# Performance work log

Hardware: AMD Instinct MI355X
Metric: run time of the kernel (lower is better)

Reference implementation:

```python
import jax, jax.numpy as jnp
import numpy as np

B, NQ, T, C = 16, 1024, 2048, 4
DIM, CDIM, H, DH = 512, 256, 1, 128
INNER = H * DH


def _rotate_half(x):
    # pairs interleaved: (..., d*2) -> (-x_odd, x_even) interleaved, matching einops '(d r)' with r=2
    x2 = x.reshape(x.shape[:-1] + (-1, 2))
    a, b = x2[..., 0], x2[..., 1]
    return jnp.stack((-b, a), axis=-1).reshape(x.shape)


def _apply_rotary(freqs, x):
    # freqs: (b, n, d) -> broadcast over heads; x: (b, h, n, d)
    f = freqs[:, None, :, :]
    return x * jnp.cos(f) + _rotate_half(x) * jnp.sin(f)


def _layernorm(x, w, b, eps=1e-5):
    mu = jnp.mean(x, axis=-1, keepdims=True)
    var = jnp.var(x, axis=-1, keepdims=True)
    return (x - mu) * jax.lax.rsqrt(var + eps) * w + b


def setup_inputs() -> dict:
    key = jax.random.key(0)
    ks = jax.random.split(key, 8)
    return dict(
        x_query=jax.random.normal(ks[0], (NQ, DIM), jnp.float32),
        x_context=jax.random.normal(ks[1], (B, T, C, CDIM), jnp.float32),
        rotary_time_emb_query=jax.random.normal(ks[2], (B, NQ, DH), jnp.float32),
        rotary_time_emb_context=jax.random.normal(ks[3], (B, T * C, DH), jnp.float32),
        context_mask=jax.random.randint(ks[4], (B, T), 0, 2) > 0,
        ln_q_w=jnp.ones((DIM,), jnp.float32), ln_q_b=jnp.zeros((DIM,), jnp.float32),
        ln_c_w=jnp.ones((CDIM,), jnp.float32), ln_c_b=jnp.zeros((CDIM,), jnp.float32),
        w_q=jax.random.normal(ks[5], (INNER, DIM), jnp.float32) / np.float32(np.sqrt(DIM)),
        w_kv=jax.random.normal(ks[6], (2 * INNER, CDIM), jnp.float32) / np.float32(np.sqrt(CDIM)),
        w_o=jax.random.normal(ks[7], (DIM, INNER), jnp.float32) / np.float32(np.sqrt(INNER)),
        b_o=jnp.zeros((DIM,), jnp.float32),
    )


def reference(x_query, x_context, rotary_time_emb_query, rotary_time_emb_context,
              context_mask, ln_q_w, ln_q_b, ln_c_w, ln_c_b, w_q, w_kv, w_o, b_o):
    b = x_context.shape[0]
    xq = _layernorm(x_query, ln_q_w, ln_q_b)                      # (NQ, DIM)
    xc = _layernorm(x_context, ln_c_w, ln_c_b)                    # (B, T, C, CDIM)
    q = xq @ w_q.T                                                # (NQ, INNER)
    q = jnp.broadcast_to(q[None], (b,) + q.shape)                 # (B, NQ, INNER)
    kv = xc @ w_kv.T                                              # (B, T, C, 2*INNER)
    k, v = jnp.split(kv, 2, axis=-1)
    k = k.reshape(b, -1, k.shape[-1])                             # (B, T*C, INNER)
    v = v.reshape(b, -1, v.shape[-1])

    def to_heads(t):  # 'b n (h d) -> b h n d'
        return t.reshape(t.shape[0], t.shape[1], H, DH).transpose(0, 2, 1, 3)

    q, k, v = to_heads(q), to_heads(k), to_heads(v)
    q = _apply_rotary(rotary_time_emb_query, q)
    k = _apply_rotary(rotary_time_emb_context, k)
    v = _apply_rotary(rotary_time_emb_context, v)                 # rotate_value=True

    # kv_mask: 'b n -> b 1 1 n' then tiled x4 along last dim (as in source)
    mask = jnp.tile(context_mask[:, None, None, :], (1, 1, 1, 4)) # (B,1,1,4T)
    scale = np.float32(1.0 / np.sqrt(DH))
    logits = jnp.einsum('bhqd,bhkd->bhqk', q, k) * scale
    logits = jnp.where(mask, logits, jnp.float32(-1e30))
    attn = jax.nn.softmax(logits, axis=-1)
    out = jnp.einsum('bhqk,bhkd->bhqd', attn, v)                  # (B,H,NQ,DH)
    out = _apply_rotary(-rotary_time_emb_query, out)              # un-rotate values
    out = out.mean(axis=2)                                        # (B, H, DH)
    return out @ w_o.T + b_o                                      # (B, H, DIM)
```

## Files before the change

### kernel.cpp

```cpp
#include <hip/hip_runtime.h>
#include <hip/hip_bf16.h>


#define DEV static __device__ __forceinline__

typedef __attribute__((ext_vector_type(4))) float f32x4;
typedef __attribute__((ext_vector_type(8))) short s16x8;
typedef __attribute__((ext_vector_type(4))) unsigned u32x4;

constexpr int NB   = 16;
constexpr int NQ   = 1024;
constexpr int SC   = 8192;
constexpr int DIM  = 512;
constexpr int CDIM = 256;
constexpr int DH   = 128;
constexpr int VTR  = 144;
constexpr int VTILE = VTR*64;

DEV short f2bf(float x){
  unsigned u = __builtin_bit_cast(unsigned, x);
  unsigned r = (u + 0x7FFFu + ((u >> 16) & 1u)) >> 16;
  return (short)r;
}

DEV unsigned pk2(float a, float b){
  unsigned short ua = __builtin_bit_cast(unsigned short, __float2bfloat16(a));
  unsigned short ub = __builtin_bit_cast(unsigned short, __float2bfloat16(b));
  return (unsigned)ua | ((unsigned)ub << 16);
}

DEV f32x4 mfma16(s16x8 a, s16x8 b, f32x4 c){
  return __builtin_amdgcn_mfma_f32_16x16x32_bf16(a, b, c, 0, 0, 0);
}

DEV void gload16(const void* g, void* l){
  __builtin_amdgcn_global_load_lds(
      (const __attribute__((address_space(1))) void*)g,
      (__attribute__((address_space(3))) void*)l, 16, 0, 0);
}

DEV s16x8 pexch(int ia0, int ia1, bool hi, unsigned L0, unsigned H0, unsigned L1, unsigned H1){
  int aL0 = __builtin_amdgcn_ds_bpermute(ia0, (int)L0);
  int aL1 = __builtin_amdgcn_ds_bpermute(ia0, (int)L1);
  int aH0 = __builtin_amdgcn_ds_bpermute(ia0, (int)H0);
  int aH1 = __builtin_amdgcn_ds_bpermute(ia0, (int)H1);
  int bL0 = __builtin_amdgcn_ds_bpermute(ia1, (int)L0);
  int bL1 = __builtin_amdgcn_ds_bpermute(ia1, (int)L1);
  int bH0 = __builtin_amdgcn_ds_bpermute(ia1, (int)H0);
  int bH1 = __builtin_amdgcn_ds_bpermute(ia1, (int)H1);
  u32x4 r;
  r[0] = (unsigned)(hi ? aL1 : aL0);
  r[1] = (unsigned)(hi ? aH1 : aH0);
  r[2] = (unsigned)(hi ? bL1 : bL0);
  r[3] = (unsigned)(hi ? bH1 : bH0);
  return __builtin_bit_cast(s16x8, r);
}

__global__ void k_cvtw(const float* __restrict__ wq, const float* __restrict__ wkv,
                       short* __restrict__ wqb, short* __restrict__ wkvb){
  int i = blockIdx.x * 256 + threadIdx.x;
  if(i < 128*512) wqb[i]  = f2bf(wq[i]);
  if(i < 256*256) wkvb[i] = f2bf(wkv[i]);
}

__global__ void k_mask(const unsigned char* __restrict__ raw, unsigned* __restrict__ bits){
  const int b = blockIdx.x, t = threadIdx.x;
  int nz = 0;
  for(int i = t; i < 8192; i += 256){
    unsigned w = ((const unsigned*)raw)[i];
    if(w & 0xFFFFFF00u) nz = 1;
  }
  int any = __syncthreads_or(nz);
  bool isInt = (any == 0);
  if(t < 64){
    unsigned out = 0;
    if(isInt){
      const int* p = (const int*)raw + (b*2048 + t*32);
      for(int j = 0; j < 32; j++) out |= (unsigned)(p[j] != 0) << j;
    } else {
      const unsigned char* p = raw + (b*2048 + t*32);
      for(int j = 0; j < 32; j++) out |= (unsigned)(p[j] != 0) << j;
    }
    bits[b*64 + t] = out;
  }
}

__global__ void k_vrow(const unsigned* __restrict__ bits, short* __restrict__ Vt){
  int b = blockIdx.y;
  int s = blockIdx.x * 256 + threadIdx.x;
  unsigned w = bits[b*64 + ((s & 2047) >> 5)];
  short v = ((w >> (s & 31)) & 1u) ? (short)0x3F80 : (short)0;
  Vt[(((size_t)b*128 + (s >> 6))*VTR + 128)*64 + (s & 63)] = v;
}

__global__ __launch_bounds__(256) void k_stats(const float* __restrict__ xc,
                                               float* __restrict__ MU, float* __restrict__ RS){
  const size_t row = (size_t)blockIdx.x * 16 + (threadIdx.x >> 4);
  const int cl = (threadIdx.x & 15) * 16;
  const float* rp = xc + row * CDIM + cl;
  float s = 0.f, sq = 0.f;
  #pragma unroll
  for(int i = 0; i < 4; i++){
    f32x4 a = *(const f32x4*)(rp + i*4);
    #pragma unroll
    for(int j = 0; j < 4; j++){ s += a[j]; sq += a[j]*a[j]; }
  }
  #pragma unroll
  for(int o = 8; o > 0; o >>= 1){ s += __shfl_xor(s, o); sq += __shfl_xor(sq, o); }
  if((threadIdx.x & 15) == 0){
    float m = s * (1.f/CDIM);
    MU[row] = m;
    RS[row] = rsqrtf(sq * (1.f/CDIM) - m*m + 1e-5f);
  }
}

__global__ __launch_bounds__(256) void k_qproj(const float* __restrict__ xq,
                                               const float* __restrict__ lnw, const float* __restrict__ lnb,
                                               const short* __restrict__ wqb, float* __restrict__ Q0){
  const int wid = threadIdx.x >> 6, lane = threadIdx.x & 63;
  const int g = lane >> 4, li = lane & 15;
  const int row0 = blockIdx.x * 64 + wid * 16;

  float mean = 0.f, rstd = 0.f;
  #pragma unroll
  for(int r = 0; r < 16; r++){
    const float* rp = xq + (row0 + r) * DIM;
    f32x4 a = *(const f32x4*)(rp + lane*8);
    f32x4 b = *(const f32x4*)(rp + lane*8 + 4);
    float s = 0.f, sq = 0.f;
    #pragma unroll
    for(int i = 0; i < 4; i++){ s += a[i] + b[i]; sq += a[i]*a[i] + b[i]*b[i]; }
    #pragma unroll
    for(int o = 32; o > 0; o >>= 1){ s += __shfl_xor(s, o); sq += __shfl_xor(sq, o); }
    if(li == r){
      mean = s / DIM;
      float var = sq / DIM - mean*mean;
      rstd = rsqrtf(var + 1e-5f);
    }
  }

  f32x4 acc[8];
  #pragma unroll
  for(int n = 0; n < 8; n++) acc[n] = f32x4{0.f,0.f,0.f,0.f};

  for(int kc = 0; kc < 16; kc++){
    int kd = kc*32 + g*8;
    const float* rp = xq + (row0 + li)*DIM + kd;
    f32x4 a0 = *(const f32x4*)rp;
    f32x4 a1 = *(const f32x4*)(rp + 4);
    f32x4 w0 = *(const f32x4*)(lnw + kd), w1 = *(const f32x4*)(lnw + kd + 4);
    f32x4 b0 = *(const f32x4*)(lnb + kd), b1 = *(const f32x4*)(lnb + kd + 4);
    s16x8 af;
    #pragma unroll
    for(int i = 0; i < 4; i++){
      af[i]   = f2bf((a0[i] - mean)*rstd*w0[i] + b0[i]);
      af[i+4] = f2bf((a1[i] - mean)*rstd*w1[i] + b1[i]);
    }
    #pragma unroll
    for(int n = 0; n < 8; n++){
      s16x8 bf = *(const s16x8*)(wqb + (n*16 + li)*DIM + kd);
      acc[n] = mfma16(af, bf, acc[n]);
    }
  }
  #pragma unroll
  for(int n = 0; n < 8; n++)
    #pragma unroll
    for(int r = 0; r < 4; r++){
      int m = row0 + g*4 + r;
      Q0[m*DH + n*16 + li] = acc[n][r];
    }
}

__global__ __launch_bounds__(512, 4) void k_kvproj(const float* __restrict__ xc,
                                                   const float* __restrict__ lnw, const float* __restrict__ lnb,
                                                   const short* __restrict__ wkvb, const float* __restrict__ rc,
                                                   const unsigned* __restrict__ bits,
                                                   const float* __restrict__ MU, const float* __restrict__ RS,
                                                   short* __restrict__ Kd, short* __restrict__ Vt){
  __shared__ __align__(16) short Klds[128][136];
  __shared__ __align__(16) short Vtlds[128][136];
  const int wid = threadIdx.x >> 6, lane = threadIdx.x & 63;
  const int g = lane >> 4, li = lane & 15;
  const int wk = wid & 3;
  const int isV = wid >> 2;
  const int b = blockIdx.y;
  const int s0 = blockIdx.x * 128;
  const int ws0 = s0 + wk * 32;

  float mean_s[2], rstd_s[2];
  #pragma unroll
  for(int sub = 0; sub < 2; sub++){
    size_t row = (size_t)b*SC + ws0 + sub*16 + li;
    mean_s[sub] = MU[row];
    rstd_s[sub] = RS[row];
  }

  f32x4 acc[8][2];
  #pragma unroll
  for(int n = 0; n < 8; n++){ acc[n][0] = f32x4{0.f,0.f,0.f,0.f}; acc[n][1] = f32x4{0.f,0.f,0.f,0.f}; }

  for(int kc = 0; kc < 8; kc++){
    int kd = kc*32 + g*8;
    f32x4 w0 = *(const f32x4*)(lnw + kd), w1 = *(const f32x4*)(lnw + kd + 4);
    f32x4 b0 = *(const f32x4*)(lnb + kd), b1 = *(const f32x4*)(lnb + kd + 4);
    s16x8 af[2];
    #pragma unroll
    for(int sub = 0; sub < 2; sub++){
      const float* rp = xc + ((size_t)b*SC + ws0 + sub*16 + li)*CDIM + kd;
      f32x4 a0 = *(const f32x4*)rp;
      f32x4 a1 = *(const f32x4*)(rp + 4);
      float mn = mean_s[sub], rs = rstd_s[sub];
      #pragma unroll
      for(int i = 0; i < 4; i++){
        af[sub][i]   = f2bf((a0[i]-mn)*rs*w0[i] + b0[i]);
        af[sub][i+4] = f2bf((a1[i]-mn)*rs*w1[i] + b1[i]);
      }
    }
    #pragma unroll
    for(int ntl = 0; ntl < 8; ntl++){
      const int nt = isV*8 + ntl;
      s16x8 bf = *(const s16x8*)(wkvb + (nt*16 + li)*CDIM + kd);
      acc[ntl][0] = mfma16(af[0], bf, acc[ntl][0]);
      acc[ntl][1] = mfma16(af[1], bf, acc[ntl][1]);
    }
  }

  if(isV == 0){
    #pragma unroll
    for(int ntl = 0; ntl < 8; ntl++)
      #pragma unroll
      for(int sub = 0; sub < 2; sub++)
        #pragma unroll
        for(int r = 0; r < 4; r++){
          int srow = wk*32 + sub*16 + g*4 + r;
          int d = ntl*16 + li;
          float f = rc[((size_t)b*SC + s0 + srow)*DH + d];
          float sn, cs; __sincosf(f, &sn, &cs);
          float kv = acc[ntl][sub][r];
          float kp = __shfl_xor(kv, 1);
          float ky = (d & 1) ? (kv*cs + kp*sn) : (kv*cs - kp*sn);
          Klds[srow][d] = f2bf(ky);
        }
  } else {
    #pragma unroll
    for(int ntl = 0; ntl < 8; ntl++)
      #pragma unroll
      for(int sub = 0; sub < 2; sub++)
        #pragma unroll
        for(int r = 0; r < 4; r++){
          int srow = wk*32 + sub*16 + g*4 + r;
          int d = ntl*16 + li;
          float f = rc[((size_t)b*SC + s0 + srow)*DH + d];
          float sn, cs; __sincosf(f, &sn, &cs);
          float vv = acc[ntl][sub][r];
          float vp = __shfl_xor(vv, 1);
          float vy = (d & 1) ? (vv*cs + vp*sn) : (vv*cs - vp*sn);
          Vtlds[d][srow] = f2bf(vy);
        }
  }
  __syncthreads();
  for(int c = threadIdx.x; c < 2048; c += 512){
    int row = c >> 4, col = (c & 15) * 8;
    s16x8 kv = *(const s16x8*)&Klds[row][col];
    *(s16x8*)(Kd + ((size_t)b*SC + s0 + row)*DH + col) = kv;
    s16x8 vv = *(const s16x8*)&Vtlds[row][col];
    int sa = s0 + col;
    unsigned w = bits[b*64 + ((sa & 2047) >> 5)];
    unsigned mb = (w >> (sa & 31)) & 0xFFu;
    #pragma unroll
    for(int j = 0; j < 8; j++) if(!((mb >> j) & 1u)) vv[j] = 0;
    *(s16x8*)(Vt + (((size_t)b*128 + (sa >> 6))*VTR + row)*64 + (sa & 63)) = vv;
  }
}

__global__ __launch_bounds__(512, 4) void k_attn(const float* __restrict__ Q0, const float* __restrict__ rq,
                                                 const short* __restrict__ Kd, const short* __restrict__ Vt,
                                                 float* __restrict__ AOp, float* __restrict__ ML){
  __shared__ __align__(16) short Kbuf[2][64*128];
  __shared__ __align__(16) short Vbuf[2][VTR*64];
  const int wid = threadIdx.x >> 6, lane = threadIdx.x & 63;
  const int g = lane >> 4, li = lane & 15;
  const int xcd = blockIdx.x & 7, ii = blockIdx.x >> 3;
  const int b  = xcd*2 + (ii >> 5);
  const int kq = (ii >> 3) & 3;
  const int qt = ii & 7;
  const int qw0 = qt*128 + wid*16;
  constexpr float C2 = 0.08838834764831845f * 1.4426950408889634f;

  s16x8 qf[4];
  {
    int qrow = qw0 + li;
    #pragma unroll
    for(int c = 0; c < 4; c++){
      int d0 = c*32 + g*8;
      const float* qp = Q0 + qrow*DH + d0;
      const float* fp = rq + ((size_t)b*NQ + qrow)*DH + d0;
      f32x4 x0 = *(const f32x4*)qp,     x1 = *(const f32x4*)(qp+4);
      f32x4 f0 = *(const f32x4*)fp,     f1 = *(const f32x4*)(fp+4);
      float xs[8] = {x0[0],x0[1],x0[2],x0[3],x1[0],x1[1],x1[2],x1[3]};
      float fs[8] = {f0[0],f0[1],f0[2],f0[3],f1[0],f1[1],f1[2],f1[3]};
      #pragma unroll
      for(int i = 0; i < 4; i++){
        float se, ce, so, co;
        __sincosf(fs[2*i],   &se, &ce);
        __sincosf(fs[2*i+1], &so, &co);
        qf[c][2*i]   = f2bf((xs[2*i]*ce   - xs[2*i+1]*se) * C2);
        qf[c][2*i+1] = f2bf((xs[2*i+1]*co + xs[2*i]*so) * C2);
      }
    }
  }

  float mrun = -1e30f;
  f32x4 acc[9];
  #pragma unroll
  for(int dt = 0; dt < 9; dt++) acc[dt] = f32x4{0.f,0.f,0.f,0.f};

  const char* Kg = (const char*)(Kd + ((size_t)b*SC + kq*2048)*DH);
  const char* Vg = (const char*)(Vt + ((size_t)b*128 + kq*32)*VTILE);

  const int ia0 = (((lane >> 4) & 1) * 32 + li) << 2;
  const int ia1 = ia0 + 64;
  const bool hi = (g >= 2);

  #define STAGE(bufi, t) do{                                                   \
    const char* Ksrc = Kg + (size_t)(t)*64*256;                                \
    _Pragma("unroll")                                                          \
    for(int j = 0; j < 2; j++){                                                \
      int rp = wid*8 + j*4 + (lane >> 4);                                      \
      int bi = ((lane & 15)*16) ^ ((rp & 7) << 4);                             \
      gload16(Ksrc + rp*256 + bi, &Kbuf[bufi][(wid*8 + j*4)*128]);             \
    }                                                                          \
    const char* Vsrc = Vg + (size_t)(t)*VTILE*2;                               \
    _Pragma("unroll")                                                          \
    for(int j = 0; j < 2; j++){                                                \
      int rp = wid*16 + j*8 + (lane >> 3);                                     \
      int bi = ((lane & 7)*16) ^ ((rp & 7) << 4);                              \
      gload16(Vsrc + rp*128 + bi, &Vbuf[bufi][(wid*16 + j*8)*64]);             \
    }                                                                          \
    if(wid < 2){                                                               \
      int rp = 128 + wid*8 + (lane >> 3);                                      \
      int bi = ((lane & 7)*16) ^ ((rp & 7) << 4);                              \
      gload16(Vsrc + rp*128 + bi, &Vbuf[bufi][(128 + wid*8)*64]);              \
    }                                                                          \
  }while(0)

  STAGE(0, 0);
  __syncthreads();

  for(int t = 0; t < 32; ++t){
    const int cur = t & 1;
    if(t < 31) STAGE(cur^1, t+1);

    f32x4 st[4];
    __builtin_amdgcn_s_setprio(1);
    #pragma unroll
    for(int ks = 0; ks < 4; ks++){
      s16x8 kf[4];
      #pragma unroll
      for(int c = 0; c < 4; c++){
        int row = ks*16 + li;
        int off = row*256 + ((c*64 + g*16) ^ ((row & 7) << 4));
        kf[c] = *(const s16x8*)((const char*)&Kbuf[cur][0] + off);
      }
      f32x4 s = f32x4{0.f,0.f,0.f,0.f};
      #pragma unroll
      for(int c = 0; c < 4; c++) s = mfma16(kf[c], qf[c], s);
      st[ks] = s;
    }
    __builtin_amdgcn_s_setprio(0);

    s16x8 pf[2];
    {
      float mt = -1e30f;
      #pragma unroll
      for(int ks = 0; ks < 4; ks++)
        #pragma unroll
        for(int r = 0; r < 4; r++) mt = fmaxf(mt, st[ks][r]);
      mt = fmaxf(mt, __shfl_xor(mt, 16));
      mt = fmaxf(mt, __shfl_xor(mt, 32));
      if(__any(mt > mrun + 3.0f)){
        float mnew = fmaxf(mrun, mt);
        float a = exp2f(mrun - mnew);
        mrun = mnew;
        #pragma unroll
        for(int dt = 0; dt < 9; dt++) acc[dt] = acc[dt] * a;
      }
      float m = mrun;
      #pragma unroll
      for(int h2 = 0; h2 < 2; h2++){
        unsigned L0 = pk2(exp2f(st[2*h2][0] - m),   exp2f(st[2*h2][1] - m));
        unsigned H0 = pk2(exp2f(st[2*h2][2] - m),   exp2f(st[2*h2][3] - m));
        unsigned L1 = pk2(exp2f(st[2*h2+1][0] - m), exp2f(st[2*h2+1][1] - m));
        unsigned H1 = pk2(exp2f(st[2*h2+1][2] - m), exp2f(st[2*h2+1][3] - m));
        pf[h2] = pexch(ia0, ia1, hi, L0, H0, L1, H1);
      }
    }

    __builtin_amdgcn_s_setprio(1);
    #pragma unroll
    for(int dt = 0; dt < 9; dt++){
      int row = dt*16 + li;
      #pragma unroll
      for(int k32 = 0; k32 < 2; k32++){
        int off = row*128 + ((k32*64 + g*16) ^ ((row & 7) << 4));
        s16x8 vf = *(const s16x8*)((const char*)&Vbuf[cur][0] + off);
        acc[dt] = mfma16(vf, pf[k32], acc[dt]);
      }
    }
    __builtin_amdgcn_s_setprio(0);

    __syncthreads();
  }

  const size_t pbase = ((size_t)kq*NB + b)*NQ;
  if(lane < 16){
    size_t o = pbase + qw0 + li;
    ML[o*2]   = mrun;
    ML[o*2+1] = acc[8][0];
  }
  {
    size_t o = (pbase + qw0 + li)*DH;
    #pragma unroll
    for(int dt = 0; dt < 8; dt++)
      *(f32x4*)(AOp + o + dt*16 + g*4) = acc[dt];
  }
}

__global__ __launch_bounds__(256) void k_fin1(const float* __restrict__ AOp, const float* __restrict__ ML,
                                              const float* __restrict__ rq, float* __restrict__ part){
  __shared__ float red[2][128];
  const int b = blockIdx.y, ch = blockIdx.x;
  const int t = threadIdx.x;
  const int d = t & 127, h = t >> 7;
  float acc = 0.f;
  #pragma unroll 2
  for(int i = 0; i < 8; i++){
    int n = ch*16 + h*8 + i;
    size_t qi = (size_t)b*NQ + n;
    float m[4], l[4];
    #pragma unroll
    for(int kq = 0; kq < 4; kq++){
      size_t o = (size_t)kq*NB*NQ + qi;
      m[kq] = ML[o*2]; l[kq] = ML[o*2+1];
    }
    float M = fmaxf(fmaxf(m[0], m[1]), fmaxf(m[2], m[3]));
    float w[4], L = 0.f;
    #pragma unroll
    for(int kq = 0; kq < 4; kq++){ w[kq] = exp2f(m[kq] - M); L += w[kq]*l[kq]; }
    float inv = 1.f / L;
    float O = 0.f;
    #pragma unroll
    for(int kq = 0; kq < 4; kq++) O += w[kq]*AOp[((size_t)kq*NB*NQ + qi)*DH + d];
    O *= inv;
    float P = __shfl_xor(O, 1);
    float f = rq[qi*DH + d];
    float sn, cs; __sincosf(f, &sn, &cs);
    acc += (d & 1) ? (O*cs - P*sn) : (O*cs + P*sn);
  }
  red[h][d] = acc;
  __syncthreads();
  if(h == 0) part[((size_t)b*64 + ch)*128 + d] = red[0][d] + red[1][d];
}

__global__ __launch_bounds__(256) void k_fin2(const float* __restrict__ part,
                                              const float* __restrict__ wo, const float* __restrict__ bo,
                                              float* __restrict__ out){
  __shared__ float sm[128];
  const int b = blockIdx.x, t = threadIdx.x;
  if(t < 128){
    float s = 0.f;
    for(int ch = 0; ch < 64; ch++) s += part[((size_t)b*64 + ch)*128 + t];
    sm[t] = s * (1.0f / NQ);
  }
  __syncthreads();
  for(int o = t; o < DIM; o += 256){
    float s = bo[o];
    const float* wr = wo + o*DH;
    #pragma unroll 4
    for(int j = 0; j < DH; j++) s += sm[j] * wr[j];
    out[b*DIM + o] = s;
  }
}

extern "C" void kernel_launch(void* const* d_in, const int* in_sizes, int n_in,
                              void* d_out, int out_size, void* d_ws, size_t ws_size,
                              hipStream_t stream){
  const float* xq   = (const float*)d_in[0];
  const float* xc   = (const float*)d_in[1];
  const float* rq   = (const float*)d_in[2];
  const float* rc   = (const float*)d_in[3];
  const unsigned char* mask = (const unsigned char*)d_in[4];
  const float* lnqw = (const float*)d_in[5];
  const float* lnqb = (const float*)d_in[6];
  const float* lncw = (const float*)d_in[7];
  const float* lncb = (const float*)d_in[8];
  const float* wq   = (const float*)d_in[9];
  const float* wkv  = (const float*)d_in[10];
  const float* wo   = (const float*)d_in[11];
  const float* bo   = (const float*)d_in[12];
  float* out = (float*)d_out;

  char* ws = (char*)d_ws;
  size_t off = 0;
  auto alloc = [&](size_t bytes){ void* p = ws + off; off += (bytes + 255) & ~(size_t)255; return p; };
  float*    Q0   = (float*)   alloc((size_t)NQ*DH*4);
  short*    wqb  = (short*)   alloc((size_t)128*512*2);
  short*    wkvb = (short*)   alloc((size_t)256*256*2);
  unsigned* bits = (unsigned*)alloc((size_t)NB*64*4);
  float*    MU   = (float*)   alloc((size_t)NB*SC*4);
  float*    RS   = (float*)   alloc((size_t)NB*SC*4);
  short*    Kd   = (short*)   alloc((size_t)NB*SC*DH*2);
  short*    Vt   = (short*)   alloc((size_t)NB*128*VTILE*2);
  float*    AOp  = (float*)   alloc((size_t)4*NB*NQ*DH*4);
  float*    ML   = (float*)   alloc((size_t)4*NB*NQ*2*4);
  float*    part = (float*)   alloc((size_t)NB*64*128*4);

  k_cvtw  <<<dim3(256),     dim3(256), 0, stream>>>(wq, wkv, wqb, wkvb);
  k_mask  <<<dim3(16),      dim3(256), 0, stream>>>(mask, bits);
  k_vrow  <<<dim3(32,16),   dim3(256), 0, stream>>>(bits, Vt);
  k_stats <<<dim3(NB*SC/16),dim3(256), 0, stream>>>(xc, MU, RS);
  k_qproj <<<dim3(16),      dim3(256), 0, stream>>>(xq, lnqw, lnqb, wqb, Q0);
  k_kvproj<<<dim3(64,16),   dim3(512), 0, stream>>>(xc, lncw, lncb, wkvb, rc, bits, MU, RS, Kd, Vt);
  k_attn  <<<dim3(512),     dim3(512), 0, stream>>>(Q0, rq, Kd, Vt, AOp, ML);
  k_fin1  <<<dim3(64,16),   dim3(256), 0, stream>>>(AOp, ML, rq, part);
  k_fin2  <<<dim3(16),      dim3(256), 0, stream>>>(part, wo, bo, out);
}
```

Measured before the change: 344.1 us.

## Split attention keys eight ways with 32-key tiles and bf16 partials

The attention kernel now splits each batch's keys into eight chunks instead of four, launching 1024 blocks with 32-key K/V tiles and a tighter launch-bounds occupancy hint. This is meant to fill more CUs and cut per-block shared memory. The partial outputs are stored as bf16 to halve partial-result traffic, and the combine kernel is generalised to eight chunks. The trade-offs are more partial results to merge, fewer MFMAs per barrier, possible register pressure or spills from the occupancy hint, and reduced precision in the partials.

```diff
diff --git a/kernel.cpp b/kernel.cpp
--- a/kernel.cpp
+++ b/kernel.cpp
@@ -16,11 +16,17 @@
 constexpr int DH   = 128;
 constexpr int VTR  = 144;
 constexpr int VTILE = VTR*64;
+constexpr int NKQ  = 8;
 
 DEV short f2bf(float x){
   unsigned u = __builtin_bit_cast(unsigned, x);
   unsigned r = (u + 0x7FFFu + ((u >> 16) & 1u)) >> 16;
   return (short)r;
+}
+
+DEV float bf2f(short v){
+  unsigned u = ((unsigned)(unsigned short)v) << 16;
+  return __builtin_bit_cast(float, u);
 }
 
 DEV unsigned pk2(float a, float b){
@@ -273,17 +279,18 @@
   }
 }
 
-__global__ __launch_bounds__(512, 4) void k_attn(const float* __restrict__ Q0, const float* __restrict__ rq,
+__global__ __launch_bounds__(512, 8) void k_attn(const float* __restrict__ Q0, const float* __restrict__ rq,
                                                  const short* __restrict__ Kd, const short* __restrict__ Vt,
-                                                 float* __restrict__ AOp, float* __restrict__ ML){
-  __shared__ __align__(16) short Kbuf[2][64*128];
-  __shared__ __align__(16) short Vbuf[2][VTR*64];
+                                                 short* __restrict__ AOp, float* __restrict__ ML){
+  __shared__ __align__(16) short Kbuf[2][32*128];
+  __shared__ __align__(16) short Vbuf[2][VTR*32];
   const int wid = threadIdx.x >> 6, lane = threadIdx.x & 63;
   const int g = lane >> 4, li = lane & 15;
-  const int xcd = blockIdx.x & 7, ii = blockIdx.x >> 3;
-  const int b  = xcd*2 + (ii >> 5);
-  const int kq = (ii >> 3) & 3;
-  const int qt = ii & 7;
+  const int oid = (blockIdx.x & 7) * 128 + (blockIdx.x >> 3);
+  const int b  = oid >> 6;
+  const int rem = oid & 63;
+  const int qt = rem >> 3;
+  const int kq = rem & 7;
   const int qw0 = qt*128 + wid*16;
   constexpr float C2 = 0.08838834764831845f * 1.4426950408889634f;
 
@@ -315,32 +322,28 @@
   #pragma unroll
   for(int dt = 0; dt < 9; dt++) acc[dt] = f32x4{0.f,0.f,0.f,0.f};
 
-  const char* Kg = (const char*)(Kd + ((size_t)b*SC + kq*2048)*DH);
-  const char* Vg = (const char*)(Vt + ((size_t)b*128 + kq*32)*VTILE);
+  const char* Kg = (const char*)(Kd + ((size_t)b*SC + kq*1024)*DH);
+  const char* Vg = (const char*)(Vt + ((size_t)b*128 + kq*16)*VTILE);
 
   const int ia0 = (((lane >> 4) & 1) * 32 + li) << 2;
   const int ia1 = ia0 + 64;
   const bool hi = (g >= 2);
 
   #define STAGE(bufi, t) do{                                                   \
-    const char* Ksrc = Kg + (size_t)(t)*64*256;                                \
-    _Pragma("unroll")                                                          \
-    for(int j = 0; j < 2; j++){                                                \
-      int rp = wid*8 + j*4 + (lane >> 4);                                      \
+    const char* Ksrc = Kg + (size_t)(t)*32*256;                                \
+    {                                                                          \
+      int rp = wid*4 + (lane >> 4);                                            \
       int bi = ((lane & 15)*16) ^ ((rp & 7) << 4);                             \
-      gload16(Ksrc + rp*256 + bi, &Kbuf[bufi][(wid*8 + j*4)*128]);             \
+      gload16(Ksrc + rp*256 + bi, &Kbuf[bufi][(wid*4)*128]);                   \
     }                                                                          \
-    const char* Vsrc = Vg + (size_t)(t)*VTILE*2;                               \
-    _Pragma("unroll")                                                          \
-    for(int j = 0; j < 2; j++){                                                \
-      int rp = wid*16 + j*8 + (lane >> 3);                                     \
-      int bi = ((lane & 7)*16) ^ ((rp & 7) << 4);                              \
-      gload16(Vsrc + rp*128 + bi, &Vbuf[bufi][(wid*16 + j*8)*64]);             \
+    const char* Vsrc = Vg + (size_t)((t) >> 1)*VTILE*2 + ((t) & 1)*64;         \
+    {                                                                          \
+      int rp = wid*16 + (lane >> 2);                                           \
+      gload16(Vsrc + rp*128 + (lane & 3)*16, &Vbuf[bufi][(wid*16)*32]);        \
     }                                                                          \
-    if(wid < 2){                                                               \
-      int rp = 128 + wid*8 + (lane >> 3);                                      \
-      int bi = ((lane & 7)*16) ^ ((rp & 7) << 4);                              \
-      gload16(Vsrc + rp*128 + bi, &Vbuf[bufi][(128 + wid*8)*64]);              \
+    if(wid == 0){                                                              \
+      int rp = 128 + (lane >> 2);                                              \
+      gload16(Vsrc + rp*128 + (lane & 3)*16, &Vbuf[bufi][128*32]);             \
     }                                                                          \
   }while(0)
 
@@ -351,10 +354,10 @@
     const int cur = t & 1;
     if(t < 31) STAGE(cur^1, t+1);
 
-    f32x4 st[4];
+    f32x4 st[2];
     __builtin_amdgcn_s_setprio(1);
     #pragma unroll
-    for(int ks = 0; ks < 4; ks++){
+    for(int ks = 0; ks < 2; ks++){
       s16x8 kf[4];
       #pragma unroll
       for(int c = 0; c < 4; c++){
@@ -369,11 +372,11 @@
     }
     __builtin_amdgcn_s_setprio(0);
 
-    s16x8 pf[2];
+    s16x8 pf;
     {
       float mt = -1e30f;
       #pragma unroll
-      for(int ks = 0; ks < 4; ks++)
+      for(int ks = 0; ks < 2; ks++)
         #pragma unroll
         for(int r = 0; r < 4; r++) mt = fmaxf(mt, st[ks][r]);
       mt = fmaxf(mt, __shfl_xor(mt, 16));
@@ -386,26 +389,19 @@
         for(int dt = 0; dt < 9; dt++) acc[dt] = acc[dt] * a;
       }
       float m = mrun;
-      #pragma unroll
-      for(int h2 = 0; h2 < 2; h2++){
-        unsigned L0 = pk2(exp2f(st[2*h2][0] - m),   exp2f(st[2*h2][1] - m));
-        unsigned H0 = pk2(exp2f(st[2*h2][2] - m),   exp2f(st[2*h2][3] - m));
-        unsigned L1 = pk2(exp2f(st[2*h2+1][0] - m), exp2f(st[2*h2+1][1] - m));
-        unsigned H1 = pk2(exp2f(st[2*h2+1][2] - m), exp2f(st[2*h2+1][3] - m));
-        pf[h2] = pexch(ia0, ia1, hi, L0, H0, L1, H1);
-      }
+      unsigned L0 = pk2(exp2f(st[0][0] - m), exp2f(st[0][1] - m));
+      unsigned H0 = pk2(exp2f(st[0][2] - m), exp2f(st[0][3] - m));
+      unsigned L1 = pk2(exp2f(st[1][0] - m), exp2f(st[1][1] - m));
+      unsigned H1 = pk2(exp2f(st[1][2] - m), exp2f(st[1][3] - m));
+      pf = pexch(ia0, ia1, hi, L0, H0, L1, H1);
     }
 
     __builtin_amdgcn_s_setprio(1);
     #pragma unroll
     for(int dt = 0; dt < 9; dt++){
       int row = dt*16 + li;
-      #pragma unroll
-      for(int k32 = 0; k32 < 2; k32++){
-        int off = row*128 + ((k32*64 + g*16) ^ ((row & 7) << 4));
-        s16x8 vf = *(const s16x8*)((const char*)&Vbuf[cur][0] + off);
-        acc[dt] = mfma16(vf, pf[k32], acc[dt]);
-      }
+      s16x8 vf = *(const s16x8*)&Vbuf[cur][row*32 + g*8];
+      acc[dt] = mfma16(vf, pf, acc[dt]);
     }
     __builtin_amdgcn_s_setprio(0);
 
@@ -421,12 +417,16 @@
   {
     size_t o = (pbase + qw0 + li)*DH;
     #pragma unroll
-    for(int dt = 0; dt < 8; dt++)
-      *(f32x4*)(AOp + o + dt*16 + g*4) = acc[dt];
-  }
-}
-
-__global__ __launch_bounds__(256) void k_fin1(const float* __restrict__ AOp, const float* __restrict__ ML,
+    for(int dt = 0; dt < 8; dt++){
+      uint2 pk;
+      pk.x = pk2(acc[dt][0], acc[dt][1]);
+      pk.y = pk2(acc[dt][2], acc[dt][3]);
+      *(uint2*)(AOp + o + dt*16 + g*4) = pk;
+    }
+  }
+}
+
+__global__ __launch_bounds__(256) void k_fin1(const short* __restrict__ AOp, const float* __restrict__ ML,
                                               const float* __restrict__ rq, float* __restrict__ part){
   __shared__ float red[2][128];
   const int b = blockIdx.y, ch = blockIdx.x;
@@ -437,20 +437,22 @@
   for(int i = 0; i < 8; i++){
     int n = ch*16 + h*8 + i;
     size_t qi = (size_t)b*NQ + n;
-    float m[4], l[4];
-    #pragma unroll
-    for(int kq = 0; kq < 4; kq++){
+    float m[NKQ], l[NKQ];
+    #pragma unroll
+    for(int kq = 0; kq < NKQ; kq++){
       size_t o = (size_t)kq*NB*NQ + qi;
       m[kq] = ML[o*2]; l[kq] = ML[o*2+1];
     }
-    float M = fmaxf(fmaxf(m[0], m[1]), fmaxf(m[2], m[3]));
-    float w[4], L = 0.f;
-    #pragma unroll
-    for(int kq = 0; kq < 4; kq++){ w[kq] = exp2f(m[kq] - M); L += w[kq]*l[kq]; }
+    float M = m[0];
+    #pragma unroll
+    for(int kq = 1; kq < NKQ; kq++) M = fmaxf(M, m[kq]);
+    float w[NKQ], L = 0.f;
+    #pragma unroll
+    for(int kq = 0; kq < NKQ; kq++){ w[kq] = exp2f(m[kq] - M); L += w[kq]*l[kq]; }
     float inv = 1.f / L;
     float O = 0.f;
     #pragma unroll
-    for(int kq = 0; kq < 4; kq++) O += w[kq]*AOp[((size_t)kq*NB*NQ + qi)*DH + d];
+    for(int kq = 0; kq < NKQ; kq++) O += w[kq]*bf2f(AOp[((size_t)kq*NB*NQ + qi)*DH + d]);
     O *= inv;
     float P = __shfl_xor(O, 1);
     float f = rq[qi*DH + d];
@@ -511,8 +513,8 @@
   float*    RS   = (float*)   alloc((size_t)NB*SC*4);
   short*    Kd   = (short*)   alloc((size_t)NB*SC*DH*2);
   short*    Vt   = (short*)   alloc((size_t)NB*128*VTILE*2);
-  float*    AOp  = (float*)   alloc((size_t)4*NB*NQ*DH*4);
-  float*    ML   = (float*)   alloc((size_t)4*NB*NQ*2*4);
+  short*    AOp  = (short*)   alloc((size_t)NKQ*NB*NQ*DH*2);
+  float*    ML   = (float*)   alloc((size_t)NKQ*NB*NQ*2*4);
   float*    part = (float*)   alloc((size_t)NB*64*128*4);
 
   k_cvtw  <<<dim3(256),     dim3(256), 0, stream>>>(wq, wkv, wqb, wkvb);
@@ -521,7 +523,7 @@
   k_stats <<<dim3(NB*SC/16),dim3(256), 0, stream>>>(xc, MU, RS);
   k_qproj <<<dim3(16),      dim3(256), 0, stream>>>(xq, lnqw, lnqb, wqb, Q0);
   k_kvproj<<<dim3(64,16),   dim3(512), 0, stream>>>(xc, lncw, lncb, wkvb, rc, bits, MU, RS, Kd, Vt);
-  k_attn  <<<dim3(512),     dim3(512), 0, stream>>>(Q0, rq, Kd, Vt, AOp, ML);
+  k_attn  <<<dim3(1024),    dim3(512), 0, stream>>>(Q0, rq, Kd, Vt, AOp, ML);
   k_fin1  <<<dim3(64,16),   dim3(256), 0, stream>>>(AOp, ML, rq, part);
   k_fin2  <<<dim3(16),      dim3(256), 0, stream>>>(part, wo, bo, out);
 }
```

New measurement: 639.2 us. 85.8% more time.
